# Kernel tuning notes

Hardware: AMD Instinct MI355X
Metric: run time of the kernel (lower is better)

The kernel has to match this reference:

```python
import jax, jax.numpy as jnp
import numpy as np

N_NODES = 50000
N_EDGES = 800000
IN_DIM = 128
H_DIM = 128
NUM_RELS = 8


def setup_inputs() -> dict:
    key = jax.random.key(0)
    ks = jax.random.split(key, 10)
    s_in = 1.0 / np.sqrt(IN_DIM)
    s_h = 1.0 / np.sqrt(H_DIM)
    return {
        "features": jax.random.normal(ks[0], (N_NODES, IN_DIM), jnp.float32),
        "etypes": jax.random.randint(ks[1], (N_EDGES,), 0, NUM_RELS),
        "edge_weight": jax.random.uniform(ks[2], (N_EDGES,), jnp.float32),
        "src": jax.random.randint(ks[3], (N_EDGES,), 0, N_NODES),
        "dst": jax.random.randint(ks[4], (N_EDGES,), 0, N_NODES),
        "comp1": jax.random.normal(ks[5], (NUM_RELS, NUM_RELS), jnp.float32) * (1.0 / NUM_RELS),
        "V1": jax.random.normal(ks[6], (NUM_RELS, IN_DIM, H_DIM), jnp.float32) * s_in,
        "bias1": jnp.zeros((H_DIM,), jnp.float32),
        "comp2": jax.random.normal(ks[7], (NUM_RELS, NUM_RELS), jnp.float32) * (1.0 / NUM_RELS),
        "V2": jax.random.normal(ks[8], (NUM_RELS, H_DIM, H_DIM), jnp.float32) * s_h,
        "bias2": jnp.zeros((H_DIM,), jnp.float32),
    }


def _rel_graph_conv(x, src, dst, etypes, norm, comp, V, bias):
    # Basis decomposition: W[r] = sum_b comp[r,b] * V[b]  -> [R, in, out]
    W = jnp.einsum('rb,bio->rio', comp, V)
    # Transform every node by every relation once: [N, R, out]
    H = jnp.einsum('ni,rio->nro', x, W)
    # Per-edge message: gather (src, etype), scale by edge norm
    m = H[src, etypes] * norm  # [E, out]
    # Scatter-sum to destination nodes
    agg = jax.ops.segment_sum(m, dst, num_segments=x.shape[0])
    return agg + bias


def reference(features, etypes, edge_weight, src, dst,
              comp1, V1, bias1, comp2, V2, bias2):
    norm = edge_weight[:, None]  # edge_weight.unsqueeze(1)
    h = _rel_graph_conv(features, src, dst, etypes, norm, comp1, V1, bias1)
    h = jax.nn.relu(h)
    h = _rel_graph_conv(h, src, dst, etypes, norm, comp2, V2, bias2)
    # F.dropout with training=False is identity (eval mode)
    return h
```

## Files before the change

### kernel.cpp

```cpp
#include <hip/hip_runtime.h>
#include <hip/hip_fp16.h>
#include <stdint.h>

constexpr int N_NODES = 50000;
constexpr int N_EDGES = 800000;
constexpr int HD      = 128;
constexpr int NREL    = 8;
constexpr int NBUCK   = N_NODES * NREL;

typedef unsigned short ushortT;
using bf16x8 = __attribute__((ext_vector_type(8))) short;
using f32x4  = __attribute__((ext_vector_type(4))) float;

__device__ __forceinline__ float b2f(uint32_t lo16){
  uint32_t x = lo16 << 16; float f; __builtin_memcpy(&f,&x,4); return f;
}
__device__ __forceinline__ uint16_t f2b(float f){
  uint32_t x; __builtin_memcpy(&x,&f,4);
  uint32_t r = (x + 0x7FFFu + ((x>>16)&1u)) >> 16;
  return (uint16_t)r;
}

constexpr int H_BLOCKS   = (N_EDGES + 255)/256;
constexpr int F2B_BLOCKS = (N_NODES*HD/4 + 255)/256;
__global__ void k_histprep(const int* __restrict__ dst, const int* __restrict__ et,
                           int* __restrict__ deg, int* __restrict__ pos,
                           const float* __restrict__ feat,
                           const float* __restrict__ comp1, const float* __restrict__ V1,
                           const float* __restrict__ comp2, const float* __restrict__ V2,
                           ushortT* __restrict__ xb,
                           ushortT* __restrict__ Wt1, ushortT* __restrict__ Wt2){
  if(blockIdx.x < H_BLOCKS){
    int i = blockIdx.x*256 + threadIdx.x;
    if(i<N_EDGES) pos[i] = atomicAdd(&deg[dst[i]*NREL + et[i]],1);
  } else if(blockIdx.x < H_BLOCKS + F2B_BLOCKS){
    int i = (blockIdx.x - H_BLOCKS)*256 + threadIdx.x;
    if(i < N_NODES*HD/4){
      float4 v = ((const float4*)feat)[i];
      ushort4 o;
      o.x=f2b(v.x); o.y=f2b(v.y); o.z=f2b(v.z); o.w=f2b(v.w);
      ((ushort4*)xb)[i]=o;
    }
  } else {
    int t = (blockIdx.x - H_BLOCKS - F2B_BLOCKS)*256 + threadIdx.x;
    int layer = t >> 17;
    t &= 131071;
    const float* comp = layer? comp2 : comp1;
    const float* V    = layer? V2    : V1;
    ushortT* Wt       = layer? Wt2   : Wt1;
    int o  = t >> 10;
    int rk = t & 1023;
    int r  = rk >> 7, k = rk & 127;
    float s=0.f;
    #pragma unroll
    for(int b=0;b<NREL;b++) s += comp[r*NREL+b]*V[(b<<14) + k*HD + o];
    Wt[t]=f2b(s);
  }
}

__global__ void k_scan1(const int* __restrict__ in, int* __restrict__ out,
                        int* __restrict__ part, int n){
  __shared__ int sm[256];
  int t = threadIdx.x; int i = blockIdx.x*256+t;
  int v = (i<n)? in[i] : 0;
  sm[t]=v; __syncthreads();
  for(int off=1; off<256; off<<=1){
    int x = (t>=off)? sm[t-off] : 0;
    __syncthreads();
    sm[t]+=x;
    __syncthreads();
  }
  if(i<n) out[i]=sm[t]-v;
  if(t==255) part[blockIdx.x]=sm[255];
}

__global__ void k_scanmid(int* __restrict__ part, int n){
  __shared__ int sm[256];
  __shared__ int carry;
  int t=threadIdx.x;
  if(t==0) carry=0;
  __syncthreads();
  for(int base=0; base<n; base+=256){
    int i=base+t;
    int v=(i<n)? part[i] : 0;
    sm[t]=v; __syncthreads();
    for(int off=1; off<256; off<<=1){
      int x=(t>=off)? sm[t-off] : 0;
      __syncthreads();
      sm[t]+=x;
      __syncthreads();
    }
    int tot = sm[255];
    if(i<n) part[i]=sm[t]-v+carry;
    __syncthreads();
    if(t==0) carry += tot;
    __syncthreads();
  }
}

__global__ void k_fin(const int* __restrict__ offs, const int* __restrict__ part,
                      int* __restrict__ offs_full){
  int i = blockIdx.x*blockDim.x + threadIdx.x;
  if(i < NBUCK) offs_full[i] = offs[i] + part[i>>8];
  else if(i == NBUCK) offs_full[i] = N_EDGES;
}

__global__ void k_scatter(const int* __restrict__ src, const int* __restrict__ et,
                          const float* __restrict__ w, const int* __restrict__ dst,
                          const int* __restrict__ offs_full, const int* __restrict__ pos,
                          uint32_t* __restrict__ es){
  int i = blockIdx.x*blockDim.x + threadIdx.x;
  if(i<N_EDGES){
    int b = dst[i]*NREL + et[i];
    __half h = __float2half(w[i]);
    ushortT hb; __builtin_memcpy(&hb,&h,2);
    es[offs_full[b] + pos[i]] = (uint32_t)(src[i] & 0xFFFF) | ((uint32_t)hb << 16);
  }
}

__global__ void __launch_bounds__(256)
k_agg(const ushortT* __restrict__ xb,
      const int* __restrict__ offs_full,
      const uint32_t* __restrict__ es,
      ushortT* __restrict__ Acat){
  int wave = blockIdx.x*4 + (threadIdx.x>>6);
  int lane = threadIdx.x & 63;
  int q = lane >> 4, f = lane & 15;
  int b = wave*4 + q;
  int beg = offs_full[b], cnt = offs_full[b+1] - beg;
  const uint32_t* ep = es + beg;
  float a[8] = {};
  uint32_t e = 0;
  if(cnt > 0) e = ep[0];
  for(int j=0;j<cnt;j++){
    uint32_t ce = e;
    if(j+1 < cnt) e = ep[j+1];
    ushortT hb = (ushortT)(ce >> 16);
    __half h; __builtin_memcpy(&h,&hb,2);
    float w = __half2float(h);
    int s = (int)(ce & 0xFFFFu);
    bf16x8 v = *(const bf16x8*)&xb[(size_t)s*HD + f*8];
    #pragma unroll
    for(int t=0;t<8;t++) a[t] += w * b2f((uint16_t)v[t]);
  }
  uint32_t pk[4];
  #pragma unroll
  for(int i=0;i<4;i++)
    pk[i] = (uint32_t)f2b(a[2*i]) | ((uint32_t)f2b(a[2*i+1])<<16);
  *(uint4*)&Acat[(size_t)b*HD + f*8] = *(uint4*)pk;
}

constexpr int BM=64, BN=128, BK=64, LDKG=72;
__global__ void __launch_bounds__(256)
k_gemm(const ushortT* __restrict__ A,
       const ushortT* __restrict__ Wt,
       const float* __restrict__ bias,
       float* __restrict__ outF,
       ushortT* __restrict__ outB,
       int M, int relu){
  __shared__ ushortT Asm[BM][LDKG];
  __shared__ ushortT Bsm[BN][LDKG];
  int tid = threadIdx.x;
  int wid = tid>>6, lane = tid&63;
  int l15 = lane&15, lhi = lane>>4;
  int row0 = blockIdx.x*BM;
  int wr = (wid>>1)*32, wc = (wid&1)*64;
  f32x4 acc[2][4] = {};
  for(int kt=0; kt<NREL*HD; kt+=BK){
    #pragma unroll
    for(int q=0;q<2;q++){
      int slot = q*256 + tid;
      int r = slot>>3, kb8 = (slot&7)*8;
      int grow = row0 + r; if(grow >= M) grow = M-1;
      *(bf16x8*)&Asm[r][kb8] = *(const bf16x8*)&A[(size_t)grow*1024 + kt + kb8];
    }
    #pragma unroll
    for(int q=0;q<4;q++){
      int slot = q*256 + tid;
      int c = slot>>3, kb8 = (slot&7)*8;
      *(bf16x8*)&Bsm[c][kb8] = *(const bf16x8*)&Wt[(size_t)c*1024 + kt + kb8];
    }
    __syncthreads();
    #pragma unroll
    for(int kk=0;kk<2;kk++){
      bf16x8 af[2], bfr[4];
      #pragma unroll
      for(int m=0;m<2;m++)  af[m]  = *(const bf16x8*)&Asm[wr + m*16 + l15][kk*32 + lhi*8];
      #pragma unroll
      for(int n=0;n<4;n++)  bfr[n] = *(const bf16x8*)&Bsm[wc + n*16 + l15][kk*32 + lhi*8];
      #pragma unroll
      for(int m=0;m<2;m++)
        #pragma unroll
        for(int n=0;n<4;n++)
          acc[m][n] = __builtin_amdgcn_mfma_f32_16x16x32_bf16(af[m], bfr[n], acc[m][n], 0,0,0);
    }
    __syncthreads();
  }
  #pragma unroll
  for(int m=0;m<2;m++){
    #pragma unroll
    for(int j=0;j<4;j++){
      int grow = row0 + wr + m*16 + lhi*4 + j;
      if(grow < M){
        #pragma unroll
        for(int n=0;n<4;n++){
          int col = wc + n*16 + l15;
          float v = acc[m][n][j] + bias[col];
          if(relu) v = fmaxf(v, 0.f);
          if(outF) outF[(size_t)grow*HD + col] = v;
          else     outB[(size_t)grow*HD + col] = f2b(v);
        }
      }
    }
  }
}

extern "C" void kernel_launch(void* const* d_in, const int* in_sizes, int n_in,
                              void* d_out, int out_size, void* d_ws, size_t ws_size,
                              hipStream_t stream){
  const float* feat  = (const float*)d_in[0];
  const int*   etyp  = (const int*)  d_in[1];
  const float* ew    = (const float*)d_in[2];
  const int*   src   = (const int*)  d_in[3];
  const int*   dst   = (const int*)  d_in[4];
  const float* comp1 = (const float*)d_in[5];
  const float* V1    = (const float*)d_in[6];
  const float* bias1 = (const float*)d_in[7];
  const float* comp2 = (const float*)d_in[8];
  const float* V2    = (const float*)d_in[9];
  const float* bias2 = (const float*)d_in[10];
  float* out = (float*)d_out;

  char* p = (char*)d_ws;
  auto alloc = [&](size_t bytes)->char* {
    char* q = p; p += (bytes + 255) & ~(size_t)255; return q;
  };
  ushortT* Wt1   = (ushortT*)alloc((size_t)HD*NREL*HD*2);
  ushortT* Wt2   = (ushortT*)alloc((size_t)HD*NREL*HD*2);
  ushortT* Acat  = (ushortT*)alloc((size_t)NBUCK*HD*2);
  ushortT* xb    = (ushortT*)alloc((size_t)N_NODES*HD*2);
  ushortT* hmid  = (ushortT*)alloc((size_t)N_NODES*HD*2);
  int*   deg   = (int*)  alloc((size_t)NBUCK*4);
  int*   offs  = (int*)  alloc((size_t)NBUCK*4);
  int*   offsF = (int*)  alloc((size_t)(NBUCK+1)*4);
  int*   part1 = (int*)  alloc(2048*4);
  int*   pos   = (int*)  alloc((size_t)N_EDGES*4);
  uint32_t* es = (uint32_t*)alloc((size_t)N_EDGES*4);

  hipMemsetAsync(deg, 0, (size_t)NBUCK*4, stream);
  k_histprep<<<H_BLOCKS + F2B_BLOCKS + 1024, 256, 0, stream>>>(
      dst,etyp,deg,pos, feat, comp1,V1,comp2,V2, xb, Wt1,Wt2);
  int nb1 = (NBUCK+255)/256;
  k_scan1<<<nb1,256,0,stream>>>(deg,offs,part1,NBUCK);
  k_scanmid<<<1,256,0,stream>>>(part1,nb1);
  k_fin<<<(NBUCK+256)/256 + 1,256,0,stream>>>(offs,part1,offsF);
  k_scatter<<<H_BLOCKS,256,0,stream>>>(src,etyp,ew,dst,offsF,pos,es);

  int aggGrid  = NBUCK/16;
  int gemmGrid = (N_NODES + BM - 1)/BM;
  k_agg<<<aggGrid,256,0,stream>>>(xb,   offsF, es, Acat);
  k_gemm<<<gemmGrid,256,0,stream>>>(Acat, Wt1, bias1, nullptr, hmid, N_NODES, 1);
  k_agg<<<aggGrid,256,0,stream>>>(hmid, offsF, es, Acat);
  k_gemm<<<gemmGrid,256,0,stream>>>(Acat, Wt2, bias2, out, nullptr, N_NODES, 0);
}
```

Before: 242.5 us.

## Prefetch gathered rows in aggregation and widen scan and histogram blocks

The aggregation loop now software-pipelines the source-row gather: it loads the next edge's feature vector and the edge after that ahead of the accumulate, hiding gather latency. The scan now uses 1024-element blocks and the mid-scan 512 threads, so k_scanmid has one iteration instead of several. The histogram part processes four edges per thread with fewer blocks. These changes trade extra registers and longer per-thread work for fewer dependent stalls and fewer serial scan passes.

```diff
diff --git a/kernel.cpp b/kernel.cpp
--- a/kernel.cpp
+++ b/kernel.cpp
@@ -21,7 +21,7 @@
   return (uint16_t)r;
 }
 
-constexpr int H_BLOCKS   = (N_EDGES + 255)/256;
+constexpr int H4_BLOCKS  = (N_EDGES + 1023)/1024;
 constexpr int F2B_BLOCKS = (N_NODES*HD/4 + 255)/256;
 __global__ void k_histprep(const int* __restrict__ dst, const int* __restrict__ et,
                            int* __restrict__ deg, int* __restrict__ pos,
@@ -30,11 +30,15 @@
                            const float* __restrict__ comp2, const float* __restrict__ V2,
                            ushortT* __restrict__ xb,
                            ushortT* __restrict__ Wt1, ushortT* __restrict__ Wt2){
-  if(blockIdx.x < H_BLOCKS){
-    int i = blockIdx.x*256 + threadIdx.x;
-    if(i<N_EDGES) pos[i] = atomicAdd(&deg[dst[i]*NREL + et[i]],1);
-  } else if(blockIdx.x < H_BLOCKS + F2B_BLOCKS){
-    int i = (blockIdx.x - H_BLOCKS)*256 + threadIdx.x;
+  if(blockIdx.x < H4_BLOCKS){
+    int base = blockIdx.x*1024 + threadIdx.x;
+    #pragma unroll
+    for(int u=0;u<4;u++){
+      int i = base + u*256;
+      if(i<N_EDGES) pos[i] = atomicAdd(&deg[dst[i]*NREL + et[i]],1);
+    }
+  } else if(blockIdx.x < H4_BLOCKS + F2B_BLOCKS){
+    int i = (blockIdx.x - H4_BLOCKS)*256 + threadIdx.x;
     if(i < N_NODES*HD/4){
       float4 v = ((const float4*)feat)[i];
       ushort4 o;
@@ -42,7 +46,7 @@
       ((ushort4*)xb)[i]=o;
     }
   } else {
-    int t = (blockIdx.x - H_BLOCKS - F2B_BLOCKS)*256 + threadIdx.x;
+    int t = (blockIdx.x - H4_BLOCKS - F2B_BLOCKS)*256 + threadIdx.x;
     int layer = t >> 17;
     t &= 131071;
     const float* comp = layer? comp2 : comp1;
@@ -60,37 +64,37 @@
 
 __global__ void k_scan1(const int* __restrict__ in, int* __restrict__ out,
                         int* __restrict__ part, int n){
-  __shared__ int sm[256];
-  int t = threadIdx.x; int i = blockIdx.x*256+t;
+  __shared__ int sm[1024];
+  int t = threadIdx.x; int i = blockIdx.x*1024+t;
   int v = (i<n)? in[i] : 0;
   sm[t]=v; __syncthreads();
-  for(int off=1; off<256; off<<=1){
+  for(int off=1; off<1024; off<<=1){
     int x = (t>=off)? sm[t-off] : 0;
     __syncthreads();
     sm[t]+=x;
     __syncthreads();
   }
   if(i<n) out[i]=sm[t]-v;
-  if(t==255) part[blockIdx.x]=sm[255];
+  if(t==1023) part[blockIdx.x]=sm[1023];
 }
 
 __global__ void k_scanmid(int* __restrict__ part, int n){
-  __shared__ int sm[256];
+  __shared__ int sm[512];
   __shared__ int carry;
   int t=threadIdx.x;
   if(t==0) carry=0;
   __syncthreads();
-  for(int base=0; base<n; base+=256){
+  for(int base=0; base<n; base+=512){
     int i=base+t;
     int v=(i<n)? part[i] : 0;
     sm[t]=v; __syncthreads();
-    for(int off=1; off<256; off<<=1){
+    for(int off=1; off<512; off<<=1){
       int x=(t>=off)? sm[t-off] : 0;
       __syncthreads();
       sm[t]+=x;
       __syncthreads();
     }
-    int tot = sm[255];
+    int tot = sm[511];
     if(i<n) part[i]=sm[t]-v+carry;
     __syncthreads();
     if(t==0) carry += tot;
@@ -101,7 +105,7 @@
 __global__ void k_fin(const int* __restrict__ offs, const int* __restrict__ part,
                       int* __restrict__ offs_full){
   int i = blockIdx.x*blockDim.x + threadIdx.x;
-  if(i < NBUCK) offs_full[i] = offs[i] + part[i>>8];
+  if(i < NBUCK) offs_full[i] = offs[i] + part[i>>10];
   else if(i == NBUCK) offs_full[i] = N_EDGES;
 }
 
@@ -130,18 +134,24 @@
   int beg = offs_full[b], cnt = offs_full[b+1] - beg;
   const uint32_t* ep = es + beg;
   float a[8] = {};
-  uint32_t e = 0;
-  if(cnt > 0) e = ep[0];
+  uint32_t e0 = 0, e1 = 0;
+  bf16x8 v0 = {};
+  if(cnt > 0){
+    e0 = ep[0];
+    v0 = *(const bf16x8*)&xb[(size_t)(e0 & 0xFFFFu)*HD + f*8];
+    if(cnt > 1) e1 = ep[1];
+  }
   for(int j=0;j<cnt;j++){
-    uint32_t ce = e;
-    if(j+1 < cnt) e = ep[j+1];
-    ushortT hb = (ushortT)(ce >> 16);
+    bf16x8 v1 = {};
+    if(j+1 < cnt)
+      v1 = *(const bf16x8*)&xb[(size_t)(e1 & 0xFFFFu)*HD + f*8];
+    uint32_t e2 = (j+2 < cnt)? ep[j+2] : 0;
+    ushortT hb = (ushortT)(e0 >> 16);
     __half h; __builtin_memcpy(&h,&hb,2);
     float w = __half2float(h);
-    int s = (int)(ce & 0xFFFFu);
-    bf16x8 v = *(const bf16x8*)&xb[(size_t)s*HD + f*8];
-    #pragma unroll
-    for(int t=0;t<8;t++) a[t] += w * b2f((uint16_t)v[t]);
+    #pragma unroll
+    for(int t=0;t<8;t++) a[t] += w * b2f((uint16_t)v0[t]);
+    e0 = e1; e1 = e2; v0 = v1;
   }
   uint32_t pk[4];
   #pragma unroll
@@ -247,14 +257,14 @@
   int*   pos   = (int*)  alloc((size_t)N_EDGES*4);
   uint32_t* es = (uint32_t*)alloc((size_t)N_EDGES*4);
 
-  hipMemsetAsync(deg, 0, (size_t)NBUCK*4, stream);
-  k_histprep<<<H_BLOCKS + F2B_BLOCKS + 1024, 256, 0, stream>>>(
+  (void)hipMemsetAsync(deg, 0, (size_t)NBUCK*4, stream);
+  k_histprep<<<H4_BLOCKS + F2B_BLOCKS + 1024, 256, 0, stream>>>(
       dst,etyp,deg,pos, feat, comp1,V1,comp2,V2, xb, Wt1,Wt2);
-  int nb1 = (NBUCK+255)/256;
-  k_scan1<<<nb1,256,0,stream>>>(deg,offs,part1,NBUCK);
-  k_scanmid<<<1,256,0,stream>>>(part1,nb1);
+  int nb1 = (NBUCK+1023)/1024;
+  k_scan1<<<nb1,1024,0,stream>>>(deg,offs,part1,NBUCK);
+  k_scanmid<<<1,512,0,stream>>>(part1,nb1);
   k_fin<<<(NBUCK+256)/256 + 1,256,0,stream>>>(offs,part1,offsF);
-  k_scatter<<<H_BLOCKS,256,0,stream>>>(src,etyp,ew,dst,offsF,pos,es);
+  k_scatter<<<(N_EDGES+255)/256,256,0,stream>>>(src,etyp,ew,dst,offsF,pos,es);
 
   int aggGrid  = NBUCK/16;
   int gemmGrid = (N_NODES + BM - 1)/BM;
```

Result: no change. 238.0 us (-1.9%).
